# Kernel tuning notes

Hardware: AMD Instinct MI355X
Metric: run time of the kernel (lower is better)

Reference implementation:

```python
import jax, jax.numpy as jnp
import numpy as np

N_NODES = 100000
N_EDGES = 1200000
D_FEAT = 64


def setup_inputs() -> dict:
    key = jax.random.key(0)
    k1, k2, k3 = jax.random.split(key, 3)
    feat = jax.random.normal(k1, (N_NODES, D_FEAT), dtype=jnp.float32)
    eps = jnp.zeros((1,), dtype=jnp.float32)
    edge_src = jax.random.randint(k2, (N_EDGES,), 0, N_NODES, dtype=jnp.int32)
    edge_dst = jax.random.randint(k3, (N_EDGES,), 0, N_NODES, dtype=jnp.int32)
    return {"feat": feat, "eps": eps, "edge_src": edge_src, "edge_dst": edge_dst}


def reference(feat, eps, edge_src, edge_dst):
    # DGL update_all(copy_u('h','m'), sum('m','neigh')):
    # gather source-node features along edges, segment-sum into destination nodes.
    messages = feat[edge_src]  # [E, D] gather
    neigh = jax.ops.segment_sum(messages, edge_dst, num_segments=N_NODES)  # [N, D]
    # eps-scaled residual: (1 + eps) * feat + neigh
    return (1.0 + eps) * feat + neigh
```

## Files before the change

kernel.cpp:

```cpp
#include <hip/hip_runtime.h>


#define N_NODES 100000
#define D_FEAT  64
#define N_EDGES 1200000

#define BSHIFT  6
#define NPB     64
#define KB      ((N_NODES + NPB - 1) / NPB)
#define CAP_B   1024
#define NB      256
#define EPB     ((N_EDGES + NB - 1) / NB)
#define NCAP    32
#define OVF_CAP 4096
#define SCAN_BK 32
#define CHUNK   7
#define CAST_ITEMS (N_NODES * D_FEAT / 8)
#define CAST_BLOCKS ((CAST_ITEMS + 255) / 256)

__device__ __forceinline__ unsigned short f32_to_bf16_rne(float f) {
    unsigned int u = __float_as_uint(f);
    u += 0x7fffu + ((u >> 16) & 1u);
    return (unsigned short)(u >> 16);
}
__device__ __forceinline__ float bf_lo(unsigned int q) { return __uint_as_float(q << 16); }
__device__ __forceinline__ float bf_hi(unsigned int q) { return __uint_as_float(q & 0xffff0000u); }

__global__ __launch_bounds__(256) void gin_phase1_kernel(
    const int* __restrict__ edge_dst,
    int* __restrict__ counts,
    int* __restrict__ ovf_cnt,
    const float* __restrict__ feat,
    unsigned int* __restrict__ fb)
{
    __shared__ int hist[KB];
    const int tid = threadIdx.x;
    if (blockIdx.x < NB) {
        for (int k = tid; k < KB; k += 256) hist[k] = 0;
        if (blockIdx.x == 0 && tid == 0) ovf_cnt[0] = 0;
        __syncthreads();
        const int e0 = blockIdx.x * EPB;
        const int e1 = min(e0 + EPB, N_EDGES);
        for (int e = e0 + tid; e < e1; e += 256)
            atomicAdd(&hist[edge_dst[e] >> BSHIFT], 1);
        __syncthreads();
        for (int k = tid; k < KB; k += 256)
            counts[blockIdx.x * KB + k] = hist[k];
    } else {
        const int i = (blockIdx.x - NB) * 256 + tid;
        if (i < CAST_ITEMS) {
            const float4 f0 = reinterpret_cast<const float4*>(feat)[2 * i];
            const float4 f1 = reinterpret_cast<const float4*>(feat)[2 * i + 1];
            uint4 q;
            q.x = (unsigned)f32_to_bf16_rne(f0.x) | ((unsigned)f32_to_bf16_rne(f0.y) << 16);
            q.y = (unsigned)f32_to_bf16_rne(f0.z) | ((unsigned)f32_to_bf16_rne(f0.w) << 16);
            q.z = (unsigned)f32_to_bf16_rne(f1.x) | ((unsigned)f32_to_bf16_rne(f1.y) << 16);
            q.w = (unsigned)f32_to_bf16_rne(f1.z) | ((unsigned)f32_to_bf16_rne(f1.w) << 16);
            reinterpret_cast<uint4*>(fb)[i] = q;
        }
    }
}

__global__ __launch_bounds__(256) void gin_scanA_kernel(
    const int* __restrict__ counts,
    int* __restrict__ start_T,
    int* __restrict__ btot)
{
    __shared__ int tile[SCAN_BK][NB + 1];
    const int tid  = threadIdx.x;
    const int lane = tid & 63;
    const int w    = tid >> 6;
    const int k0   = blockIdx.x * SCAN_BK;

    for (int idx = tid; idx < SCAN_BK * NB; idx += 256) {
        const int kk = idx & (SCAN_BK - 1);
        const int b  = idx >> 5;
        const int k  = k0 + kk;
        tile[kk][b] = (k < KB) ? counts[b * KB + k] : 0;
    }
    __syncthreads();
    for (int kk = w; kk < SCAN_BK; kk += 4) {
        const int base = lane * 4;
        const int v0 = tile[kk][base],     v1 = tile[kk][base + 1];
        const int v2 = tile[kk][base + 2], v3 = tile[kk][base + 3];
        const int s = v0 + v1 + v2 + v3;
        int incl = s;
        #pragma unroll
        for (int off = 1; off < 64; off <<= 1) {
            const int t = __shfl_up(incl, off);
            if (lane >= off) incl += t;
        }
        const int excl = incl - s;
        tile[kk][base]     = excl;
        tile[kk][base + 1] = excl + v0;
        tile[kk][base + 2] = excl + v0 + v1;
        tile[kk][base + 3] = excl + v0 + v1 + v2;
        if (lane == 63 && k0 + kk < KB) btot[k0 + kk] = incl;
    }
    __syncthreads();
    for (int idx = tid; idx < SCAN_BK * NB; idx += 256) {
        const int kk = idx & (SCAN_BK - 1);
        const int b  = idx >> 5;
        const int k  = k0 + kk;
        if (k < KB) start_T[b * KB + k] = tile[kk][b];
    }
}

__global__ __launch_bounds__(256) void gin_place_kernel(
    const int* __restrict__ edge_src,
    const int* __restrict__ edge_dst,
    const int* __restrict__ counts,
    const int* __restrict__ start_T,
    int* __restrict__ buckets,
    int* __restrict__ ovf_cnt,
    int* __restrict__ ovf)
{
    __shared__ int ent[EPB];
    __shared__ int gp[EPB];
    __shared__ int cur[KB];
    __shared__ int goff[KB];
    __shared__ int tsum[256];
    const int tid = threadIdx.x;
    const int b = blockIdx.x;

    const int kbase = tid * CHUNK;
    int c[CHUNK];
    int mysum = 0;
    #pragma unroll
    for (int i = 0; i < CHUNK; ++i) {
        const int k = kbase + i;
        c[i] = (k < KB) ? counts[b * KB + k] : 0;
        mysum += c[i];
    }
    tsum[tid] = mysum;
    __syncthreads();
    for (int off = 1; off < 256; off <<= 1) {
        const int v = (tid >= off) ? tsum[tid - off] : 0;
        __syncthreads();
        tsum[tid] += v;
        __syncthreads();
    }
    int excl = tsum[tid] - mysum;
    #pragma unroll
    for (int i = 0; i < CHUNK; ++i) {
        const int k = kbase + i;
        if (k < KB) {
            cur[k]  = excl;
            goff[k] = k * CAP_B + start_T[b * KB + k] - excl;
        }
        excl += c[i];
    }
    __syncthreads();

    const int e0 = b * EPB;
    const int e1 = min(e0 + EPB, N_EDGES);
    for (int e = e0 + tid; e < e1; e += 256) {
        const int dst = edge_dst[e];
        const int src = edge_src[e];
        const int k = dst >> BSHIFT;
        const int t = atomicAdd(&cur[k], 1);
        const int g = goff[k] + t;
        ent[t] = src | ((dst & (NPB - 1)) << 17);
        if (g - k * CAP_B < CAP_B) {
            gp[t] = g;
        } else {
            gp[t] = -1;
            const int o = atomicAdd(ovf_cnt, 1);
            if (o < OVF_CAP) { ovf[2 * o] = src; ovf[2 * o + 1] = dst; }
        }
    }
    __syncthreads();

    const int ne = e1 - e0;
    for (int i = tid; i < ne; i += 256) {
        const int g = gp[i];
        if (g >= 0) buckets[g] = ent[i];
    }
}

__global__ __launch_bounds__(256) void gin_gather_kernel(
    const float* __restrict__ feat,
    const unsigned int* __restrict__ fb,
    const float* __restrict__ eps,
    const int* __restrict__ btot,
    const int* __restrict__ buckets,
    int* __restrict__ ovf_cnt,
    int* __restrict__ ovf,
    float* __restrict__ out)
{
    __shared__ int lcnt[NPB];
    __shared__ int sl[NPB * NCAP];
    const int tid  = threadIdx.x;
    const int k    = blockIdx.x;
    const int lane = tid & 63;
    const int w    = tid >> 6;

    if (tid < NPB) lcnt[tid] = 0;
    __syncthreads();

    int m = btot[k];
    if (m > CAP_B) m = CAP_B;
    const int* __restrict__ bkt = buckets + k * CAP_B;
    for (int i = tid; i < m; i += 256) {
        const int e  = bkt[i];
        const int ld = e >> 17;
        const int t  = atomicAdd(&lcnt[ld], 1);
        if (t < NCAP) sl[ld * NCAP + t] = e & 0x1FFFF;
        else {
            const int o = atomicAdd(ovf_cnt, 1);
            if (o < OVF_CAP) { ovf[2 * o] = e & 0x1FFFF; ovf[2 * o + 1] = k * NPB + ld; }
        }
    }
    __syncthreads();

    const int r = lane >> 4;
    const int c = lane & 15;
    const float scale = 1.0f + eps[0];
    const int node_base = k * NPB;

    for (int nl = w * 16; nl < w * 16 + 16; nl += 2) {
        const int nodeA = node_base + nl;
        const int nodeB = nodeA + 1;
        int nA = lcnt[nl];     if (nA > NCAP) nA = NCAP;
        int nB = lcnt[nl + 1]; if (nB > NCAP) nB = NCAP;
        const int myA = sl[nl * NCAP + (lane & (NCAP - 1))];
        const int myB = sl[(nl + 1) * NCAP + (lane & (NCAP - 1))];

        float a0 = 0.f, a1 = 0.f, a2 = 0.f, a3 = 0.f;
        float b0 = 0.f, b1 = 0.f, b2 = 0.f, b3 = 0.f;
        const int nmax = (nA > nB) ? nA : nB;
        for (int j0 = 0; j0 < nmax; j0 += 4) {
            const int j  = j0 + r;
            const int jA = (j < nA) ? j : 0;
            const int jB = (j < nB) ? j : 0;
            const int sA = __shfl(myA, jA);
            const int sB = __shfl(myB, jB);
            if (j < nA) {
                const uint2 q = *reinterpret_cast<const uint2*>(&fb[sA * (D_FEAT / 2) + c * 2]);
                a0 += bf_lo(q.x); a1 += bf_hi(q.x);
                a2 += bf_lo(q.y); a3 += bf_hi(q.y);
            }
            if (j < nB) {
                const uint2 q = *reinterpret_cast<const uint2*>(&fb[sB * (D_FEAT / 2) + c * 2]);
                b0 += bf_lo(q.x); b1 += bf_hi(q.x);
                b2 += bf_lo(q.y); b3 += bf_hi(q.y);
            }
        }
        a0 += __shfl_xor(a0, 16); b0 += __shfl_xor(b0, 16);
        a1 += __shfl_xor(a1, 16); b1 += __shfl_xor(b1, 16);
        a2 += __shfl_xor(a2, 16); b2 += __shfl_xor(b2, 16);
        a3 += __shfl_xor(a3, 16); b3 += __shfl_xor(b3, 16);
        a0 += __shfl_xor(a0, 32); b0 += __shfl_xor(b0, 32);
        a1 += __shfl_xor(a1, 32); b1 += __shfl_xor(b1, 32);
        a2 += __shfl_xor(a2, 32); b2 += __shfl_xor(b2, 32);
        a3 += __shfl_xor(a3, 32); b3 += __shfl_xor(b3, 32);

        if (r == 0) {
            if (nodeA < N_NODES) {
                const float4 f = *reinterpret_cast<const float4*>(&feat[nodeA * D_FEAT + c * 4]);
                float4 o;
                o.x = scale * f.x + a0; o.y = scale * f.y + a1;
                o.z = scale * f.z + a2; o.w = scale * f.w + a3;
                *reinterpret_cast<float4*>(&out[nodeA * D_FEAT + c * 4]) = o;
            }
            if (nodeB < N_NODES) {
                const float4 f = *reinterpret_cast<const float4*>(&feat[nodeB * D_FEAT + c * 4]);
                float4 o;
                o.x = scale * f.x + b0; o.y = scale * f.y + b1;
                o.z = scale * f.z + b2; o.w = scale * f.w + b3;
                *reinterpret_cast<float4*>(&out[nodeB * D_FEAT + c * 4]) = o;
            }
        }
    }
}

__global__ __launch_bounds__(256) void gin_cleanup_kernel(
    const float* __restrict__ feat,
    const int* __restrict__ ovf_cnt,
    const int* __restrict__ ovf,
    float* __restrict__ out)
{
    int m = ovf_cnt[0];
    if (m > OVF_CAP) m = OVF_CAP;
    const int d = threadIdx.x & 63;
    for (int e = threadIdx.x >> 6; e < m; e += 4) {
        const int src = ovf[2 * e], dst = ovf[2 * e + 1];
        atomicAdd(&out[dst * D_FEAT + d], feat[src * D_FEAT + d]);
    }
}

__global__ __launch_bounds__(256) void gin_init_kernel(
    const float* __restrict__ feat, const float* __restrict__ eps, float* __restrict__ out)
{
    const float scale = 1.0f + eps[0];
    int i = blockIdx.x * blockDim.x + threadIdx.x;
    if (i < (N_NODES * D_FEAT) / 4) {
        float4 v = reinterpret_cast<const float4*>(feat)[i];
        v.x *= scale; v.y *= scale; v.z *= scale; v.w *= scale;
        reinterpret_cast<float4*>(out)[i] = v;
    }
}
__global__ __launch_bounds__(256) void gin_scatter_kernel(
    const float* __restrict__ feat, const int* __restrict__ edge_src,
    const int* __restrict__ edge_dst, float* __restrict__ out)
{
    const int edge = blockIdx.x * 4 + (threadIdx.x >> 6);
    const int lane = threadIdx.x & 63;
    if (edge < N_EDGES)
        atomicAdd(&out[edge_dst[edge] * D_FEAT + lane], feat[edge_src[edge] * D_FEAT + lane]);
}

extern "C" void kernel_launch(void* const* d_in, const int* in_sizes, int n_in,
                              void* d_out, int out_size, void* d_ws, size_t ws_size,
                              hipStream_t stream)
{
    const float* feat     = (const float*)d_in[0];
    const float* eps      = (const float*)d_in[1];
    const int*   edge_src = (const int*)d_in[2];
    const int*   edge_dst = (const int*)d_in[3];
    float* out = (float*)d_out;

    const size_t fb_ints  = (size_t)N_NODES * D_FEAT / 2;
    const size_t cnt_ints = (size_t)NB * KB;
    const size_t bkt_ints = (size_t)KB * CAP_B;
    const size_t need = sizeof(int) *
        (fb_ints + 2 * cnt_ints + KB + 16 + 2 * OVF_CAP + bkt_ints);
    if (ws_size >= need) {
        unsigned int* fb = (unsigned int*)d_ws;
        int* counts  = (int*)(fb + fb_ints);
        int* start_T = counts + cnt_ints;
        int* btot    = start_T + cnt_ints;
        int* ovf_cnt = btot + KB;
        int* ovf     = ovf_cnt + 16;
        int* buckets = ovf + 2 * OVF_CAP;

        gin_phase1_kernel<<<NB + CAST_BLOCKS, 256, 0, stream>>>(
            edge_dst, counts, ovf_cnt, feat, fb);
        gin_scanA_kernel<<<(KB + SCAN_BK - 1) / SCAN_BK, 256, 0, stream>>>(
            counts, start_T, btot);
        gin_place_kernel<<<NB, 256, 0, stream>>>(
            edge_src, edge_dst, counts, start_T, buckets, ovf_cnt, ovf);
        gin_gather_kernel<<<KB, 256, 0, stream>>>(
            feat, fb, eps, btot, buckets, ovf_cnt, ovf, out);
        gin_cleanup_kernel<<<1, 256, 0, stream>>>(feat, ovf_cnt, ovf, out);
    } else {
        const int total4 = (N_NODES * D_FEAT) / 4;
        gin_init_kernel<<<(total4 + 255) / 256, 256, 0, stream>>>(feat, eps, out);
        gin_scatter_kernel<<<(N_EDGES + 3) / 4, 256, 0, stream>>>(
            feat, edge_src, edge_dst, out);
    }
}
```

Measured before the change: 157.3 us.

## Replace histogram-scan-place bucketing with global atomic slot claiming in one kernel

Drops the three-pass counting sort (per-block histogram, transpose scan, place) and instead has each edge claim a bucket slot with a global atomicAdd on a padded per-bucket counter, writing directly into the fixed-capacity bucket. The cast-to-bf16 work stays fused in the same launch, and a memset zeroes the counters and the overflow counter. This removes two kernel launches and the count/start arrays, at the cost of contended global atomics and unordered bucket contents.

```diff
diff --git a/kernel.cpp b/kernel.cpp
--- a/kernel.cpp
+++ b/kernel.cpp
@@ -9,14 +9,14 @@
 #define NPB     64
 #define KB      ((N_NODES + NPB - 1) / NPB)
 #define CAP_B   1024
-#define NB      256
-#define EPB     ((N_EDGES + NB - 1) / NB)
 #define NCAP    32
 #define OVF_CAP 4096
-#define SCAN_BK 32
-#define CHUNK   7
+#define CNT_STRIDE 16
 #define CAST_ITEMS (N_NODES * D_FEAT / 8)
 #define CAST_BLOCKS ((CAST_ITEMS + 255) / 256)
+#define PLACE_BLOCKS 1536
+#define PLACE_THREADS (PLACE_BLOCKS * 256)
+#define EDGE_UNROLL 4
 
 __device__ __forceinline__ unsigned short f32_to_bf16_rne(float f) {
     unsigned int u = __float_as_uint(f);
@@ -26,28 +26,46 @@
 __device__ __forceinline__ float bf_lo(unsigned int q) { return __uint_as_float(q << 16); }
 __device__ __forceinline__ float bf_hi(unsigned int q) { return __uint_as_float(q & 0xffff0000u); }
 
-__global__ __launch_bounds__(256) void gin_phase1_kernel(
+__global__ __launch_bounds__(256) void gin_cast_place_kernel(
+    const float* __restrict__ feat,
+    const int* __restrict__ edge_src,
     const int* __restrict__ edge_dst,
-    int* __restrict__ counts,
+    unsigned int* __restrict__ fb,
+    int* __restrict__ bcnt,
     int* __restrict__ ovf_cnt,
-    const float* __restrict__ feat,
-    unsigned int* __restrict__ fb)
-{
-    __shared__ int hist[KB];
+    int* __restrict__ ovf,
+    int* __restrict__ buckets)
+{
     const int tid = threadIdx.x;
-    if (blockIdx.x < NB) {
-        for (int k = tid; k < KB; k += 256) hist[k] = 0;
-        if (blockIdx.x == 0 && tid == 0) ovf_cnt[0] = 0;
-        __syncthreads();
-        const int e0 = blockIdx.x * EPB;
-        const int e1 = min(e0 + EPB, N_EDGES);
-        for (int e = e0 + tid; e < e1; e += 256)
-            atomicAdd(&hist[edge_dst[e] >> BSHIFT], 1);
-        __syncthreads();
-        for (int k = tid; k < KB; k += 256)
-            counts[blockIdx.x * KB + k] = hist[k];
+    if (blockIdx.x < PLACE_BLOCKS) {
+        const int gid = blockIdx.x * 256 + tid;
+        int src[EDGE_UNROLL], dst[EDGE_UNROLL], slot[EDGE_UNROLL];
+        bool valid[EDGE_UNROLL];
+        #pragma unroll
+        for (int u = 0; u < EDGE_UNROLL; ++u) {
+            const int e = gid + u * PLACE_THREADS;
+            valid[u] = (e < N_EDGES);
+            if (valid[u]) { dst[u] = edge_dst[e]; src[u] = edge_src[e]; }
+        }
+        #pragma unroll
+        for (int u = 0; u < EDGE_UNROLL; ++u) {
+            if (valid[u])
+                slot[u] = atomicAdd(&bcnt[(dst[u] >> BSHIFT) * CNT_STRIDE], 1);
+        }
+        #pragma unroll
+        for (int u = 0; u < EDGE_UNROLL; ++u) {
+            if (valid[u]) {
+                const int k = dst[u] >> BSHIFT;
+                if (slot[u] < CAP_B) {
+                    buckets[k * CAP_B + slot[u]] = src[u] | ((dst[u] & (NPB - 1)) << 17);
+                } else {
+                    const int o = atomicAdd(ovf_cnt, 1);
+                    if (o < OVF_CAP) { ovf[2 * o] = src[u]; ovf[2 * o + 1] = dst[u]; }
+                }
+            }
+        }
     } else {
-        const int i = (blockIdx.x - NB) * 256 + tid;
+        const int i = (blockIdx.x - PLACE_BLOCKS) * 256 + tid;
         if (i < CAST_ITEMS) {
             const float4 f0 = reinterpret_cast<const float4*>(feat)[2 * i];
             const float4 f1 = reinterpret_cast<const float4*>(feat)[2 * i + 1];
@@ -61,128 +79,11 @@
     }
 }
 
-__global__ __launch_bounds__(256) void gin_scanA_kernel(
-    const int* __restrict__ counts,
-    int* __restrict__ start_T,
-    int* __restrict__ btot)
-{
-    __shared__ int tile[SCAN_BK][NB + 1];
-    const int tid  = threadIdx.x;
-    const int lane = tid & 63;
-    const int w    = tid >> 6;
-    const int k0   = blockIdx.x * SCAN_BK;
-
-    for (int idx = tid; idx < SCAN_BK * NB; idx += 256) {
-        const int kk = idx & (SCAN_BK - 1);
-        const int b  = idx >> 5;
-        const int k  = k0 + kk;
-        tile[kk][b] = (k < KB) ? counts[b * KB + k] : 0;
-    }
-    __syncthreads();
-    for (int kk = w; kk < SCAN_BK; kk += 4) {
-        const int base = lane * 4;
-        const int v0 = tile[kk][base],     v1 = tile[kk][base + 1];
-        const int v2 = tile[kk][base + 2], v3 = tile[kk][base + 3];
-        const int s = v0 + v1 + v2 + v3;
-        int incl = s;
-        #pragma unroll
-        for (int off = 1; off < 64; off <<= 1) {
-            const int t = __shfl_up(incl, off);
-            if (lane >= off) incl += t;
-        }
-        const int excl = incl - s;
-        tile[kk][base]     = excl;
-        tile[kk][base + 1] = excl + v0;
-        tile[kk][base + 2] = excl + v0 + v1;
-        tile[kk][base + 3] = excl + v0 + v1 + v2;
-        if (lane == 63 && k0 + kk < KB) btot[k0 + kk] = incl;
-    }
-    __syncthreads();
-    for (int idx = tid; idx < SCAN_BK * NB; idx += 256) {
-        const int kk = idx & (SCAN_BK - 1);
-        const int b  = idx >> 5;
-        const int k  = k0 + kk;
-        if (k < KB) start_T[b * KB + k] = tile[kk][b];
-    }
-}
-
-__global__ __launch_bounds__(256) void gin_place_kernel(
-    const int* __restrict__ edge_src,
-    const int* __restrict__ edge_dst,
-    const int* __restrict__ counts,
-    const int* __restrict__ start_T,
-    int* __restrict__ buckets,
-    int* __restrict__ ovf_cnt,
-    int* __restrict__ ovf)
-{
-    __shared__ int ent[EPB];
-    __shared__ int gp[EPB];
-    __shared__ int cur[KB];
-    __shared__ int goff[KB];
-    __shared__ int tsum[256];
-    const int tid = threadIdx.x;
-    const int b = blockIdx.x;
-
-    const int kbase = tid * CHUNK;
-    int c[CHUNK];
-    int mysum = 0;
-    #pragma unroll
-    for (int i = 0; i < CHUNK; ++i) {
-        const int k = kbase + i;
-        c[i] = (k < KB) ? counts[b * KB + k] : 0;
-        mysum += c[i];
-    }
-    tsum[tid] = mysum;
-    __syncthreads();
-    for (int off = 1; off < 256; off <<= 1) {
-        const int v = (tid >= off) ? tsum[tid - off] : 0;
-        __syncthreads();
-        tsum[tid] += v;
-        __syncthreads();
-    }
-    int excl = tsum[tid] - mysum;
-    #pragma unroll
-    for (int i = 0; i < CHUNK; ++i) {
-        const int k = kbase + i;
-        if (k < KB) {
-            cur[k]  = excl;
-            goff[k] = k * CAP_B + start_T[b * KB + k] - excl;
-        }
-        excl += c[i];
-    }
-    __syncthreads();
-
-    const int e0 = b * EPB;
-    const int e1 = min(e0 + EPB, N_EDGES);
-    for (int e = e0 + tid; e < e1; e += 256) {
-        const int dst = edge_dst[e];
-        const int src = edge_src[e];
-        const int k = dst >> BSHIFT;
-        const int t = atomicAdd(&cur[k], 1);
-        const int g = goff[k] + t;
-        ent[t] = src | ((dst & (NPB - 1)) << 17);
-        if (g - k * CAP_B < CAP_B) {
-            gp[t] = g;
-        } else {
-            gp[t] = -1;
-            const int o = atomicAdd(ovf_cnt, 1);
-            if (o < OVF_CAP) { ovf[2 * o] = src; ovf[2 * o + 1] = dst; }
-        }
-    }
-    __syncthreads();
-
-    const int ne = e1 - e0;
-    for (int i = tid; i < ne; i += 256) {
-        const int g = gp[i];
-        if (g >= 0) buckets[g] = ent[i];
-    }
-}
-
 __global__ __launch_bounds__(256) void gin_gather_kernel(
     const float* __restrict__ feat,
     const unsigned int* __restrict__ fb,
     const float* __restrict__ eps,
-    const int* __restrict__ btot,
+    const int* __restrict__ bcnt,
     const int* __restrict__ buckets,
     int* __restrict__ ovf_cnt,
     int* __restrict__ ovf,
@@ -198,7 +99,7 @@
     if (tid < NPB) lcnt[tid] = 0;
     __syncthreads();
 
-    int m = btot[k];
+    int m = bcnt[k * CNT_STRIDE];
     if (m > CAP_B) m = CAP_B;
     const int* __restrict__ bkt = buckets + k * CAP_B;
     for (int i = tid; i < m; i += 256) {
@@ -320,28 +221,24 @@
     const int*   edge_dst = (const int*)d_in[3];
     float* out = (float*)d_out;
 
-    const size_t fb_ints  = (size_t)N_NODES * D_FEAT / 2;
-    const size_t cnt_ints = (size_t)NB * KB;
-    const size_t bkt_ints = (size_t)KB * CAP_B;
+    const size_t fb_ints   = (size_t)N_NODES * D_FEAT / 2;
+    const size_t bcnt_ints = (size_t)KB * CNT_STRIDE;
+    const size_t bkt_ints  = (size_t)KB * CAP_B;
     const size_t need = sizeof(int) *
-        (fb_ints + 2 * cnt_ints + KB + 16 + 2 * OVF_CAP + bkt_ints);
+        (fb_ints + bcnt_ints + 16 + 2 * OVF_CAP + bkt_ints);
     if (ws_size >= need) {
         unsigned int* fb = (unsigned int*)d_ws;
-        int* counts  = (int*)(fb + fb_ints);
-        int* start_T = counts + cnt_ints;
-        int* btot    = start_T + cnt_ints;
-        int* ovf_cnt = btot + KB;
+        int* bcnt    = (int*)(fb + fb_ints);
+        int* ovf_cnt = bcnt + bcnt_ints;
         int* ovf     = ovf_cnt + 16;
         int* buckets = ovf + 2 * OVF_CAP;
 
-        gin_phase1_kernel<<<NB + CAST_BLOCKS, 256, 0, stream>>>(
-            edge_dst, counts, ovf_cnt, feat, fb);
-        gin_scanA_kernel<<<(KB + SCAN_BK - 1) / SCAN_BK, 256, 0, stream>>>(
-            counts, start_T, btot);
-        gin_place_kernel<<<NB, 256, 0, stream>>>(
-            edge_src, edge_dst, counts, start_T, buckets, ovf_cnt, ovf);
+        hipMemsetAsync(bcnt, 0, (bcnt_ints + 16) * sizeof(int), stream);
+
+        gin_cast_place_kernel<<<PLACE_BLOCKS + CAST_BLOCKS, 256, 0, stream>>>(
+            feat, edge_src, edge_dst, fb, bcnt, ovf_cnt, ovf, buckets);
         gin_gather_kernel<<<KB, 256, 0, stream>>>(
-            feat, fb, eps, btot, buckets, ovf_cnt, ovf, out);
+            feat, fb, eps, bcnt, buckets, ovf_cnt, ovf, out);
         gin_cleanup_kernel<<<1, 256, 0, stream>>>(feat, ovf_cnt, ovf, out);
     } else {
         const int total4 = (N_NODES * D_FEAT) / 4;
```

Measured after the change: 186.3 us. +18.4%, slower.
